# Kernel tuning notes

Measured on AMD Instinct MI355X. Metric: run time of the kernel, lower is better.

Reference implementation:

```python
import jax, jax.numpy as jnp
import numpy as np

D_MODEL = 2048
NUM_HEADS = 32
NUM_KV_HEADS = 8
D_K = D_MODEL // NUM_HEADS
BATCH = 2
SEQ = 2048


def setup_inputs() -> dict:
    key = jax.random.key(0)
    ks = jax.random.split(key, 9)
    s_in = 1.0 / np.sqrt(D_MODEL)
    kv_dim = NUM_KV_HEADS * D_K
    return {
        "x": jax.random.normal(ks[0], (BATCH, SEQ, D_MODEL), jnp.float32),
        "Wq": jax.random.uniform(ks[1], (D_MODEL, D_MODEL), jnp.float32, -s_in, s_in),
        "bq": jax.random.uniform(ks[2], (D_MODEL,), jnp.float32, -s_in, s_in),
        "Wk": jax.random.uniform(ks[3], (D_MODEL, kv_dim), jnp.float32, -s_in, s_in),
        "bk": jax.random.uniform(ks[4], (kv_dim,), jnp.float32, -s_in, s_in),
        "Wv": jax.random.uniform(ks[5], (D_MODEL, kv_dim), jnp.float32, -s_in, s_in),
        "bv": jax.random.uniform(ks[6], (kv_dim,), jnp.float32, -s_in, s_in),
        "Wo": jax.random.uniform(ks[7], (D_MODEL, D_MODEL), jnp.float32, -s_in, s_in),
        "bo": jax.random.uniform(ks[8], (D_MODEL,), jnp.float32, -s_in, s_in),
    }


def reference(x, Wq, bq, Wk, bk, Wv, bv, Wo, bo):
    b, s, _ = x.shape
    rep = NUM_HEADS // NUM_KV_HEADS
    # projections
    q = (x @ Wq + bq).reshape(b, s, NUM_HEADS, D_K).transpose(0, 2, 1, 3)      # [b,h,s,d]
    k = (x @ Wk + bk).reshape(b, s, NUM_KV_HEADS, D_K).transpose(0, 2, 1, 3)   # [b,g,s,d]
    v = (x @ Wv + bv).reshape(b, s, NUM_KV_HEADS, D_K).transpose(0, 2, 1, 3)
    # repeat_interleave over kv heads (head h uses kv head h // rep)
    k = jnp.repeat(k, rep, axis=1)  # [b,h,s,d]
    v = jnp.repeat(v, rep, axis=1)
    scale = 1.0 / np.sqrt(D_K).astype(np.float32)
    scores = jnp.einsum("bhqd,bhkd->bhqk", q, k) * scale
    probs = jax.nn.softmax(scores, axis=-1)
    ctx = jnp.einsum("bhqk,bhkd->bhqd", probs, v)        # [b,h,s,d]
    ctx = ctx.transpose(0, 2, 1, 3).reshape(b, s, D_MODEL)
    return ctx @ Wo + bo
```

## Files before the change

### kernel.cpp

```cpp
#include <hip/hip_runtime.h>
#include <hip/hip_bf16.h>
#include <cstdint>

#define D_MODEL 2048
#define NHEADS 32
#define NKV 8
#define DK 64
#define BATCH 2
#define SEQ 2048
#define M_TOT (BATCH * SEQ)
#define KV_DIM (NKV * DK)
#define QSCALE 0.18033688011112042f
#define MSUB 20.0f

typedef __attribute__((ext_vector_type(8))) short short8;
typedef __attribute__((ext_vector_type(4))) short short4_;
typedef __attribute__((ext_vector_type(2))) float f32x2;
typedef __attribute__((ext_vector_type(4))) float f32x4;
typedef __attribute__((ext_vector_type(16))) float f32x16;
typedef unsigned short u16;
typedef unsigned int u32;

__device__ __forceinline__ u16 f2bf(float f) {
  u32 u = __builtin_bit_cast(u32, f);
  u += 0x7fffu + ((u >> 16) & 1u);
  return (u16)(u >> 16);
}

__device__ __forceinline__ u32 cvtpk(float a, float b) {
  u32 r;
  asm("v_cvt_pk_bf16_f32 %0, %1, %2" : "=v"(r) : "v"(a), "v"(b));
  return r;
}

__device__ __forceinline__ float exp2v(float x) {
  float r;
  asm("v_exp_f32 %0, %1" : "=v"(r) : "v"(x));
  return r;
}

__device__ __forceinline__ f32x2 pkadd(f32x2 a, f32x2 b) {
  f32x2 r;
  asm("v_pk_add_f32 %0, %1, %2" : "=v"(r) : "v"(a), "v"(b));
  return r;
}

__device__ __forceinline__ void gld_lds16(const u16* g, u16* l) {
  __builtin_amdgcn_global_load_lds((__attribute__((address_space(1))) void*)g,
                                   (__attribute__((address_space(3))) void*)l,
                                   16, 0, 0);
}

__global__ void k_convert(const float* __restrict__ in, u16* __restrict__ out, int n4) {
  int i = blockIdx.x * blockDim.x + threadIdx.x;
  if (i >= n4) return;
  float4 v = reinterpret_cast<const float4*>(in)[i];
  uint2 o;
  o.x = (u32)f2bf(v.x) | ((u32)f2bf(v.y) << 16);
  o.y = (u32)f2bf(v.z) | ((u32)f2bf(v.w) << 16);
  reinterpret_cast<uint2*>(out)[i] = o;
}

__global__ void k_transpose(const float* __restrict__ W, u16* __restrict__ Wt,
                            int K, int N) {
  __shared__ float tile[32][33];
  int n0 = blockIdx.x * 32, k0 = blockIdx.y * 32;
  int tx = threadIdx.x, ty = threadIdx.y;
#pragma unroll
  for (int j = 0; j < 4; ++j)
    tile[ty + j * 8][tx] = W[(size_t)(k0 + ty + j * 8) * N + n0 + tx];
  __syncthreads();
#pragma unroll
  for (int j = 0; j < 4; ++j)
    Wt[(size_t)(n0 + ty + j * 8) * K + k0 + tx] = f2bf(tile[tx][ty + j * 8]);
}

__global__ __launch_bounds__(256) void k_gemm_qkv(
    const u16* __restrict__ A, const u16* __restrict__ Bt,
    const float* __restrict__ bq, const float* __restrict__ bk,
    const float* __restrict__ bv,
    u16* __restrict__ Qb, u16* __restrict__ Kb, u16* __restrict__ Vtr) {
  __shared__ u16 Alds[128 * 32];
  __shared__ u16 Blds[128 * 32];
  const int tid = threadIdx.x;
  const int lane = tid & 63;
  const int wid = tid >> 6;
  const int wr = wid >> 1, wc = wid & 1;
  const int l15 = lane & 15, lg = lane >> 4;
  const int row0 = blockIdx.y * 128, col0 = blockIdx.x * 128;

  f32x4 acc[4][4];
#pragma unroll
  for (int m = 0; m < 4; ++m)
#pragma unroll
    for (int n = 0; n < 4; ++n) acc[m][n] = (f32x4){0.f, 0.f, 0.f, 0.f};

  for (int k0 = 0; k0 < D_MODEL; k0 += 32) {
    __syncthreads();
#pragma unroll
    for (int s = 0; s < 2; ++s) {
      int idx = tid + s * 256;
      int r = idx >> 2;
      int c8 = (idx & 3) * 8;
      gld_lds16(A + (size_t)(row0 + r) * D_MODEL + k0 + c8, Alds + idx * 8);
      gld_lds16(Bt + (size_t)(col0 + r) * D_MODEL + k0 + c8, Blds + idx * 8);
    }
    __syncthreads();

    short8 af[4], bfm[4];
    const int ko = lg * 8;
#pragma unroll
    for (int m = 0; m < 4; ++m)
      af[m] = *(const short8*)(Alds + (wr * 64 + m * 16 + l15) * 32 + ko);
#pragma unroll
    for (int n = 0; n < 4; ++n)
      bfm[n] = *(const short8*)(Blds + (wc * 64 + n * 16 + l15) * 32 + ko);
#pragma unroll
    for (int m = 0; m < 4; ++m)
#pragma unroll
      for (int n = 0; n < 4; ++n)
        acc[m][n] = __builtin_amdgcn_mfma_f32_16x16x32_bf16(af[m], bfm[n], acc[m][n], 0, 0, 0);
  }

  if (col0 < 2048) {
#pragma unroll
    for (int m = 0; m < 4; ++m)
#pragma unroll
      for (int n = 0; n < 4; ++n) {
        int col = col0 + wc * 64 + n * 16 + l15;
        float bb = bq[col];
#pragma unroll
        for (int j = 0; j < 4; ++j) {
          int row = row0 + wr * 64 + m * 16 + lg * 4 + j;
          Qb[(size_t)row * D_MODEL + col] = f2bf((acc[m][n][j] + bb) * QSCALE);
        }
      }
  } else if (col0 < 2560) {
#pragma unroll
    for (int m = 0; m < 4; ++m)
#pragma unroll
      for (int n = 0; n < 4; ++n) {
        int ck = col0 - 2048 + wc * 64 + n * 16 + l15;
        float bb = bk[ck];
#pragma unroll
        for (int j = 0; j < 4; ++j) {
          int row = row0 + wr * 64 + m * 16 + lg * 4 + j;
          Kb[(size_t)row * KV_DIM + ck] = f2bf(acc[m][n][j] + bb);
        }
      }
  } else {
#pragma unroll
    for (int m = 0; m < 4; ++m)
#pragma unroll
      for (int n = 0; n < 4; ++n) {
        int dv = col0 - 2560 + wc * 64 + n * 16 + l15;
        float bb = bv[dv];
        int rowb = row0 + wr * 64 + m * 16 + lg * 4;
        short4_ w;
#pragma unroll
        for (int j = 0; j < 4; ++j) w[j] = (short)f2bf(acc[m][n][j] + bb);
        *(short4_*)(Vtr + (size_t)dv * M_TOT + rowb) = w;
      }
  }
}

__global__ __launch_bounds__(256) void k_gemm_out(
    const u16* __restrict__ A, const u16* __restrict__ Bt,
    const float* __restrict__ bias, float* __restrict__ Cout) {
  __shared__ u16 Alds[128 * 32];
  __shared__ u16 Blds[128 * 32];
  const int tid = threadIdx.x;
  const int lane = tid & 63;
  const int wid = tid >> 6;
  const int wr = wid >> 1, wc = wid & 1;
  const int l15 = lane & 15, lg = lane >> 4;
  const int row0 = blockIdx.y * 128, col0 = blockIdx.x * 128;

  f32x4 acc[4][4];
#pragma unroll
  for (int m = 0; m < 4; ++m)
#pragma unroll
    for (int n = 0; n < 4; ++n) acc[m][n] = (f32x4){0.f, 0.f, 0.f, 0.f};

  for (int k0 = 0; k0 < D_MODEL; k0 += 32) {
    __syncthreads();
#pragma unroll
    for (int s = 0; s < 2; ++s) {
      int idx = tid + s * 256;
      int r = idx >> 2;
      int c8 = (idx & 3) * 8;
      gld_lds16(A + (size_t)(row0 + r) * D_MODEL + k0 + c8, Alds + idx * 8);
      gld_lds16(Bt + (size_t)(col0 + r) * D_MODEL + k0 + c8, Blds + idx * 8);
    }
    __syncthreads();

    short8 af[4], bfm[4];
    const int ko = lg * 8;
#pragma unroll
    for (int m = 0; m < 4; ++m)
      af[m] = *(const short8*)(Alds + (wr * 64 + m * 16 + l15) * 32 + ko);
#pragma unroll
    for (int n = 0; n < 4; ++n)
      bfm[n] = *(const short8*)(Blds + (wc * 64 + n * 16 + l15) * 32 + ko);
#pragma unroll
    for (int m = 0; m < 4; ++m)
#pragma unroll
      for (int n = 0; n < 4; ++n)
        acc[m][n] = __builtin_amdgcn_mfma_f32_16x16x32_bf16(af[m], bfm[n], acc[m][n], 0, 0, 0);
  }

#pragma unroll
  for (int m = 0; m < 4; ++m)
#pragma unroll
    for (int n = 0; n < 4; ++n) {
      int col = col0 + wc * 64 + n * 16 + l15;
      float bb = bias[col];
#pragma unroll
      for (int j = 0; j < 4; ++j) {
        int row = row0 + wr * 64 + m * 16 + lg * 4 + j;
        Cout[(size_t)row * D_MODEL + col] = acc[m][n][j] + bb;
      }
    }
}

__global__ __launch_bounds__(512) void k_attn(
    const u16* __restrict__ Qb, const u16* __restrict__ Kb,
    const u16* __restrict__ Vt, u16* __restrict__ Ctx) {
  __shared__ u16 smem[4 * 4096];
  const int tid = threadIdx.x;
  const int lane = tid & 63;
  const int wid = tid >> 6;
  const int l31 = lane & 31;
  const int hi = lane >> 5;
  const bool ishi = hi != 0;
  const int b = blockIdx.z, h = blockIdx.y, g = h >> 2;
  const int qrow = blockIdx.x * 256 + wid * 32 + l31;
  const size_t tok = (size_t)b * SEQ + qrow;

  short8 qf[4];
  const u16* qp = Qb + tok * D_MODEL + h * DK + hi * 8;
#pragma unroll
  for (int d = 0; d < 4; ++d) qf[d] = *(const short8*)(qp + d * 16);

  f32x16 oacc0, oacc1;
#pragma unroll
  for (int i = 0; i < 16; ++i) { oacc0[i] = 0.f; oacc1[i] = 0.f; }
  float lrun = 0.f;

  char* sm = (char*)smem;
  const u16* Ksrc = Kb + (size_t)b * SEQ * KV_DIM + g * DK;
  const u16* Vsrc = Vt + (size_t)g * DK * M_TOT + b * SEQ;

#define STAGE(CUR, KV0) do {                                                   \
  int r_ = tid >> 3, c_ = tid & 7, cg_ = c_ ^ (r_ & 7);                        \
  gld_lds16(Ksrc + (size_t)((KV0) + r_) * KV_DIM + cg_ * 8,                    \
            smem + (CUR) * 4096 + tid * 8);                                    \
  gld_lds16(Vsrc + (size_t)r_ * M_TOT + (KV0) + cg_ * 8,                       \
            smem + 8192 + (CUR) * 4096 + tid * 8);                             \
} while (0)

  STAGE(0, 0);

  for (int t = 0; t < SEQ / 64; ++t) {
    const int cur = t & 1;
    __syncthreads();
    if (t + 1 < SEQ / 64) STAGE(cur ^ 1, (t + 1) * 64);

    f32x16 sacc0, sacc1;
#pragma unroll
    for (int i = 0; i < 16; ++i) { sacc0[i] = 0.f; sacc1[i] = 0.f; }
    const char* kbase = sm + cur * 8192;
    const int r0 = l31, r1 = 32 + l31;
    __builtin_amdgcn_s_setprio(1);
#pragma unroll
    for (int d = 0; d < 4; ++d) {
      short8 k0 = *(const short8*)(kbase + r0 * 128 + (((d * 2 + hi) ^ (r0 & 7)) * 16));
      short8 k1 = *(const short8*)(kbase + r1 * 128 + (((d * 2 + hi) ^ (r1 & 7)) * 16));
      sacc0 = __builtin_amdgcn_mfma_f32_32x32x16_bf16(k0, qf[d], sacc0, 0, 0, 0);
      sacc1 = __builtin_amdgcn_mfma_f32_32x32x16_bf16(k1, qf[d], sacc1, 0, 0, 0);
    }
    __builtin_amdgcn_s_setprio(0);

    float pe0[16], pe1[16];
    f32x2 sum2 = (f32x2){0.f, 0.f};
    const f32x2 negM = (f32x2){-MSUB, -MSUB};
#pragma unroll
    for (int i = 0; i < 8; ++i) {
      f32x2 a0 = pkadd((f32x2){sacc0[2 * i], sacc0[2 * i + 1]}, negM);
      f32x2 a1 = pkadd((f32x2){sacc1[2 * i], sacc1[2 * i + 1]}, negM);
      pe0[2 * i] = exp2v(a0[0]);
      pe0[2 * i + 1] = exp2v(a0[1]);
      pe1[2 * i] = exp2v(a1[0]);
      pe1[2 * i + 1] = exp2v(a1[1]);
      sum2 = pkadd(sum2, (f32x2){pe0[2 * i], pe0[2 * i + 1]});
      sum2 = pkadd(sum2, (f32x2){pe1[2 * i], pe1[2 * i + 1]});
    }
    float s32 = sum2[0] + sum2[1];
    s32 += __shfl_xor(s32, 32);
    lrun += s32;

    const char* vbase = sm + 16384 + cur * 8192;

#define PV_STEP(PE, RB, KB) do {                                               \
  u32 A_ = cvtpk(PE[(RB) + 0], PE[(RB) + 1]);                                  \
  u32 B_ = cvtpk(PE[(RB) + 4], PE[(RB) + 5]);                                  \
  u32 C_ = cvtpk(PE[(RB) + 2], PE[(RB) + 3]);                                  \
  u32 E_ = cvtpk(PE[(RB) + 6], PE[(RB) + 7]);                                  \
  u32 Ax_ = __shfl_xor(A_, 32), Bx_ = __shfl_xor(B_, 32);                      \
  u32 Cx_ = __shfl_xor(C_, 32), Ex_ = __shfl_xor(E_, 32);                      \
  union { u32 w[4]; short8 s8; } uu_;                                          \
  uu_.w[0] = ishi ? Bx_ : A_;                                                  \
  uu_.w[1] = ishi ? Ex_ : C_;                                                  \
  uu_.w[2] = ishi ? B_ : Ax_;                                                  \
  uu_.w[3] = ishi ? E_ : Cx_;                                                  \
  short8 pf_ = uu_.s8;                                                         \
  short8 vf0_ = *(const short8*)(vbase + r0 * 128 + ((((KB) * 2 + hi) ^ (r0 & 7)) * 16)); \
  short8 vf1_ = *(const short8*)(vbase + r1 * 128 + ((((KB) * 2 + hi) ^ (r1 & 7)) * 16)); \
  __builtin_amdgcn_s_setprio(1);                                               \
  oacc0 = __builtin_amdgcn_mfma_f32_32x32x16_bf16(vf0_, pf_, oacc0, 0, 0, 0);  \
  oacc1 = __builtin_amdgcn_mfma_f32_32x32x16_bf16(vf1_, pf_, oacc1, 0, 0, 0);  \
  __builtin_amdgcn_s_setprio(0);                                               \
} while (0)

    PV_STEP(pe0, 0, 0);
    PV_STEP(pe0, 8, 1);
    PV_STEP(pe1, 0, 2);
    PV_STEP(pe1, 8, 3);
#undef PV_STEP
  }

  float rl = 1.0f / lrun;
  u16* cp = Ctx + tok * D_MODEL + h * DK;
#pragma unroll
  for (int db = 0; db < 2; ++db) {
    const f32x16& oa = db ? oacc1 : oacc0;
#pragma unroll
    for (int quad = 0; quad < 4; ++quad) {
      int dbase = db * 32 + 8 * quad + 4 * hi;
      short4_ w;
#pragma unroll
      for (int j = 0; j < 4; ++j) w[j] = (short)f2bf(oa[quad * 4 + j] * rl);
      *(short4_*)(cp + dbase) = w;
    }
  }
#undef STAGE
}

extern "C" void kernel_launch(void* const* d_in, const int* in_sizes, int n_in,
                              void* d_out, int out_size, void* d_ws, size_t ws_size,
                              hipStream_t stream) {
  const float* x  = (const float*)d_in[0];
  const float* Wq = (const float*)d_in[1];
  const float* bq = (const float*)d_in[2];
  const float* Wk = (const float*)d_in[3];
  const float* bk = (const float*)d_in[4];
  const float* Wv = (const float*)d_in[5];
  const float* bv = (const float*)d_in[6];
  const float* Wo = (const float*)d_in[7];
  const float* bo = (const float*)d_in[8];
  float* out = (float*)d_out;

  char* ws = (char*)d_ws;
  u16* xb    = (u16*)(ws);
  u16* Wqkvt = (u16*)(ws + 16777216);
  u16* Wot   = (u16*)(ws + 29360128);
  u16* Qb    = (u16*)(ws + 37748736);
  u16* Kb    = (u16*)(ws + 54525952);
  u16* Vtr   = (u16*)(ws + 58720256);
  u16* Ctx   = (u16*)(ws + 62914560);

  int n4 = M_TOT * D_MODEL / 4;
  k_convert<<<(n4 + 255) / 256, 256, 0, stream>>>(x, xb, n4);
  k_transpose<<<dim3(64, 64), dim3(32, 8), 0, stream>>>(Wq, Wqkvt, D_MODEL, D_MODEL);
  k_transpose<<<dim3(16, 64), dim3(32, 8), 0, stream>>>(Wk, Wqkvt + (size_t)2048 * D_MODEL, D_MODEL, KV_DIM);
  k_transpose<<<dim3(16, 64), dim3(32, 8), 0, stream>>>(Wv, Wqkvt + (size_t)2560 * D_MODEL, D_MODEL, KV_DIM);
  k_transpose<<<dim3(64, 64), dim3(32, 8), 0, stream>>>(Wo, Wot, D_MODEL, D_MODEL);

  k_gemm_qkv<<<dim3(24, 32), 256, 0, stream>>>(xb, Wqkvt, bq, bk, bv, Qb, Kb, Vtr);

  k_attn<<<dim3(SEQ / 256, NHEADS, BATCH), 512, 0, stream>>>(Qb, Kb, Vtr, Ctx);

  k_gemm_out<<<dim3(16, 32), 256, 0, stream>>>(Ctx, Wot, bo, out);
}
```

Before: 244.5 us.

## Double-buffer GEMM LDS tiles, swizzle block order, unify QKV/out GEMM kernels

Merges the QKV and output-projection GEMMs into one templated kernel with a double-buffered LDS pipeline, so the async global-to-LDS copy of the next K tile is issued while MFMAs run on the current one. Each iteration now has one barrier before its compute instead of a load/sync/compute/sync sequence. Block IDs are remapped so adjacent workgroups take different row tiles, which is meant to improve L2 reuse of the B matrix, and launch bounds now ask for 4 blocks per CU. LDS per block doubles, which may limit occupancy.

Result: faster. 225.9 us (-7.6%).

```diff
diff --git a/kernel.cpp b/kernel.cpp
--- a/kernel.cpp
+++ b/kernel.cpp
@@ -75,19 +75,29 @@
     Wt[(size_t)(n0 + ty + j * 8) * K + k0 + tx] = f2bf(tile[tx][ty + j * 8]);
 }
 
-__global__ __launch_bounds__(256) void k_gemm_qkv(
+template <int MODE, int NBX, int NWG>
+__global__ __launch_bounds__(256, 4) void k_gemm128(
     const u16* __restrict__ A, const u16* __restrict__ Bt,
-    const float* __restrict__ bq, const float* __restrict__ bk,
-    const float* __restrict__ bv,
-    u16* __restrict__ Qb, u16* __restrict__ Kb, u16* __restrict__ Vtr) {
-  __shared__ u16 Alds[128 * 32];
-  __shared__ u16 Blds[128 * 32];
+    const float* __restrict__ b0, const float* __restrict__ b1,
+    const float* __restrict__ b2,
+    u16* __restrict__ O0, u16* __restrict__ O1, u16* __restrict__ O2,
+    float* __restrict__ Of) {
+  __shared__ u16 Alds[2][128 * 32];
+  __shared__ u16 Blds[2][128 * 32];
   const int tid = threadIdx.x;
   const int lane = tid & 63;
   const int wid = tid >> 6;
   const int wr = wid >> 1, wc = wid & 1;
   const int l15 = lane & 15, lg = lane >> 4;
-  const int row0 = blockIdx.y * 128, col0 = blockIdx.x * 128;
+  const int bid = blockIdx.x;
+  const int swz = (bid & 7) * (NWG / 8) + (bid >> 3);
+  const int by = swz / NBX, bx = swz % NBX;
+  const int row0 = by * 128, col0 = bx * 128;
+
+  const u16* pa0 = A  + (size_t)(row0 + (tid >> 2)) * D_MODEL + (tid & 3) * 8;
+  const u16* pa1 = pa0 + (size_t)64 * D_MODEL;
+  const u16* pb0 = Bt + (size_t)(col0 + (tid >> 2)) * D_MODEL + (tid & 3) * 8;
+  const u16* pb1 = pb0 + (size_t)64 * D_MODEL;
 
   f32x4 acc[4][4];
 #pragma unroll
@@ -95,44 +105,64 @@
 #pragma unroll
     for (int n = 0; n < 4; ++n) acc[m][n] = (f32x4){0.f, 0.f, 0.f, 0.f};
 
-  for (int k0 = 0; k0 < D_MODEL; k0 += 32) {
+#define GSTAGE(CUR, KOFF) do {                                                 \
+  gld_lds16(pa0 + (KOFF), &Alds[CUR][tid * 8]);                                \
+  gld_lds16(pa1 + (KOFF), &Alds[CUR][(tid + 256) * 8]);                        \
+  gld_lds16(pb0 + (KOFF), &Blds[CUR][tid * 8]);                                \
+  gld_lds16(pb1 + (KOFF), &Blds[CUR][(tid + 256) * 8]);                        \
+} while (0)
+
+#define GCOMPUTE(CUR) do {                                                     \
+  short8 af_[4], bf_[4];                                                       \
+  _Pragma("unroll")                                                            \
+  for (int m = 0; m < 4; ++m)                                                  \
+    af_[m] = *(const short8*)(&Alds[CUR][(wr * 64 + m * 16 + l15) * 32 + lg * 8]); \
+  _Pragma("unroll")                                                            \
+  for (int n = 0; n < 4; ++n)                                                  \
+    bf_[n] = *(const short8*)(&Blds[CUR][(wc * 64 + n * 16 + l15) * 32 + lg * 8]); \
+  _Pragma("unroll")                                                            \
+  for (int m = 0; m < 4; ++m)                                                  \
+    _Pragma("unroll")                                                          \
+    for (int n = 0; n < 4; ++n)                                                \
+      acc[m][n] = __builtin_amdgcn_mfma_f32_16x16x32_bf16(af_[m], bf_[n], acc[m][n], 0, 0, 0); \
+} while (0)
+
+  GSTAGE(0, 0);
+  for (int kt = 0; kt < 64; kt += 2) {
     __syncthreads();
-#pragma unroll
-    for (int s = 0; s < 2; ++s) {
-      int idx = tid + s * 256;
-      int r = idx >> 2;
-      int c8 = (idx & 3) * 8;
-      gld_lds16(A + (size_t)(row0 + r) * D_MODEL + k0 + c8, Alds + idx * 8);
-      gld_lds16(Bt + (size_t)(col0 + r) * D_MODEL + k0 + c8, Blds + idx * 8);
-    }
+    if (kt + 1 < 64) GSTAGE(1, (kt + 1) * 32);
+    GCOMPUTE(0);
     __syncthreads();
-
-    short8 af[4], bfm[4];
-    const int ko = lg * 8;
-#pragma unroll
-    for (int m = 0; m < 4; ++m)
-      af[m] = *(const short8*)(Alds + (wr * 64 + m * 16 + l15) * 32 + ko);
-#pragma unroll
-    for (int n = 0; n < 4; ++n)
-      bfm[n] = *(const short8*)(Blds + (wc * 64 + n * 16 + l15) * 32 + ko);
-#pragma unroll
-    for (int m = 0; m < 4; ++m)
-#pragma unroll
-      for (int n = 0; n < 4; ++n)
-        acc[m][n] = __builtin_amdgcn_mfma_f32_16x16x32_bf16(af[m], bfm[n], acc[m][n], 0, 0, 0);
+    if (kt + 2 < 64) GSTAGE(0, (kt + 2) * 32);
+    GCOMPUTE(1);
   }
-
-  if (col0 < 2048) {
+#undef GSTAGE
+#undef GCOMPUTE
+
+  if (MODE == 1) {
 #pragma unroll
     for (int m = 0; m < 4; ++m)
 #pragma unroll
       for (int n = 0; n < 4; ++n) {
         int col = col0 + wc * 64 + n * 16 + l15;
-        float bb = bq[col];
+        float bb = b0[col];
 #pragma unroll
         for (int j = 0; j < 4; ++j) {
           int row = row0 + wr * 64 + m * 16 + lg * 4 + j;
-          Qb[(size_t)row * D_MODEL + col] = f2bf((acc[m][n][j] + bb) * QSCALE);
+          Of[(size_t)row * D_MODEL + col] = acc[m][n][j] + bb;
+        }
+      }
+  } else if (col0 < 2048) {
+#pragma unroll
+    for (int m = 0; m < 4; ++m)
+#pragma unroll
+      for (int n = 0; n < 4; ++n) {
+        int col = col0 + wc * 64 + n * 16 + l15;
+        float bb = b0[col];
+#pragma unroll
+        for (int j = 0; j < 4; ++j) {
+          int row = row0 + wr * 64 + m * 16 + lg * 4 + j;
+          O0[(size_t)row * D_MODEL + col] = f2bf((acc[m][n][j] + bb) * QSCALE);
         }
       }
   } else if (col0 < 2560) {
@@ -141,11 +171,11 @@
 #pragma unroll
       for (int n = 0; n < 4; ++n) {
         int ck = col0 - 2048 + wc * 64 + n * 16 + l15;
-        float bb = bk[ck];
+        float bb = b1[ck];
 #pragma unroll
         for (int j = 0; j < 4; ++j) {
           int row = row0 + wr * 64 + m * 16 + lg * 4 + j;
-          Kb[(size_t)row * KV_DIM + ck] = f2bf(acc[m][n][j] + bb);
+          O1[(size_t)row * KV_DIM + ck] = f2bf(acc[m][n][j] + bb);
         }
       }
   } else {
@@ -154,73 +184,14 @@
 #pragma unroll
       for (int n = 0; n < 4; ++n) {
         int dv = col0 - 2560 + wc * 64 + n * 16 + l15;
-        float bb = bv[dv];
+        float bb = b2[dv];
         int rowb = row0 + wr * 64 + m * 16 + lg * 4;
         short4_ w;
 #pragma unroll
         for (int j = 0; j < 4; ++j) w[j] = (short)f2bf(acc[m][n][j] + bb);
-        *(short4_*)(Vtr + (size_t)dv * M_TOT + rowb) = w;
+        *(short4_*)(O2 + (size_t)dv * M_TOT + rowb) = w;
       }
   }
-}
-
-__global__ __launch_bounds__(256) void k_gemm_out(
-    const u16* __restrict__ A, const u16* __restrict__ Bt,
-    const float* __restrict__ bias, float* __restrict__ Cout) {
-  __shared__ u16 Alds[128 * 32];
-  __shared__ u16 Blds[128 * 32];
-  const int tid = threadIdx.x;
-  const int lane = tid & 63;
-  const int wid = tid >> 6;
-  const int wr = wid >> 1, wc = wid & 1;
-  const int l15 = lane & 15, lg = lane >> 4;
-  const int row0 = blockIdx.y * 128, col0 = blockIdx.x * 128;
-
-  f32x4 acc[4][4];
-#pragma unroll
-  for (int m = 0; m < 4; ++m)
-#pragma unroll
-    for (int n = 0; n < 4; ++n) acc[m][n] = (f32x4){0.f, 0.f, 0.f, 0.f};
-
-  for (int k0 = 0; k0 < D_MODEL; k0 += 32) {
-    __syncthreads();
-#pragma unroll
-    for (int s = 0; s < 2; ++s) {
-      int idx = tid + s * 256;
-      int r = idx >> 2;
-      int c8 = (idx & 3) * 8;
-      gld_lds16(A + (size_t)(row0 + r) * D_MODEL + k0 + c8, Alds + idx * 8);
-      gld_lds16(Bt + (size_t)(col0 + r) * D_MODEL + k0 + c8, Blds + idx * 8);
-    }
-    __syncthreads();
-
-    short8 af[4], bfm[4];
-    const int ko = lg * 8;
-#pragma unroll
-    for (int m = 0; m < 4; ++m)
-      af[m] = *(const short8*)(Alds + (wr * 64 + m * 16 + l15) * 32 + ko);
-#pragma unroll
-    for (int n = 0; n < 4; ++n)
-      bfm[n] = *(const short8*)(Blds + (wc * 64 + n * 16 + l15) * 32 + ko);
-#pragma unroll
-    for (int m = 0; m < 4; ++m)
-#pragma unroll
-      for (int n = 0; n < 4; ++n)
-        acc[m][n] = __builtin_amdgcn_mfma_f32_16x16x32_bf16(af[m], bfm[n], acc[m][n], 0, 0, 0);
-  }
-
-#pragma unroll
-  for (int m = 0; m < 4; ++m)
-#pragma unroll
-    for (int n = 0; n < 4; ++n) {
-      int col = col0 + wc * 64 + n * 16 + l15;
-      float bb = bias[col];
-#pragma unroll
-      for (int j = 0; j < 4; ++j) {
-        int row = row0 + wr * 64 + m * 16 + lg * 4 + j;
-        Cout[(size_t)row * D_MODEL + col] = acc[m][n][j] + bb;
-      }
-    }
 }
 
 __global__ __launch_bounds__(512) void k_attn(
@@ -376,9 +347,10 @@
   k_transpose<<<dim3(16, 64), dim3(32, 8), 0, stream>>>(Wv, Wqkvt + (size_t)2560 * D_MODEL, D_MODEL, KV_DIM);
   k_transpose<<<dim3(64, 64), dim3(32, 8), 0, stream>>>(Wo, Wot, D_MODEL, D_MODEL);
 
-  k_gemm_qkv<<<dim3(24, 32), 256, 0, stream>>>(xb, Wqkvt, bq, bk, bv, Qb, Kb, Vtr);
+  k_gemm128<0, 24, 768><<<768, 256, 0, stream>>>(xb, Wqkvt, bq, bk, bv, Qb, Kb, Vtr, nullptr);
 
   k_attn<<<dim3(SEQ / 256, NHEADS, BATCH), 512, 0, stream>>>(Qb, Kb, Vtr, Ctx);
 
-  k_gemm_out<<<dim3(16, 32), 256, 0, stream>>>(Ctx, Wot, bo, out);
-}
+  k_gemm128<1, 16, 512><<<512, 256, 0, stream>>>(Ctx, Wot, bo, nullptr, nullptr,
+                                                 nullptr, nullptr, nullptr, out);
+}
```
